# Kernel tuning notes

Measured on AMD Instinct MI355X. Metric: run time of the kernel, lower is better.

## Reference

```python
import jax, jax.numpy as jnp
import numpy as np

B, T, NODES, DEG = 16, 50, 62, 8
IN, C, H, NC, K = 64, 128, 256, 3, 5
G = B * T            # num_graphs
N = G * NODES        # total nodes
E = G * NODES * DEG  # total edges (before self loops)


def setup_inputs() -> dict:
    key = jax.random.key(0)
    ks = jax.random.split(key, 12)
    # random within-graph edges, PyG-batched with node offsets
    rng = np.random.RandomState(0)
    src = rng.randint(0, NODES, size=(G, NODES * DEG))
    dst = rng.randint(0, NODES, size=(G, NODES * DEG))
    off = (np.arange(G) * NODES)[:, None]
    edge_index = jnp.asarray(np.stack([(src + off).ravel(), (dst + off).ravel()]), dtype=jnp.int32)

    def glorot(k, shape, fan_in):
        return jax.random.normal(k, shape, jnp.float32) / np.sqrt(fan_in)

    return {
        "x": jax.random.normal(ks[0], (N, IN), jnp.float32),
        "edge_index": edge_index,
        "edge_attr": jax.random.normal(ks[1], (E, 1), jnp.float32),
        "W_l": glorot(ks[2], (IN, C), IN), "b_l": jnp.zeros((C,), jnp.float32),
        "W_r": glorot(ks[3], (IN, C), IN), "b_r": jnp.zeros((C,), jnp.float32),
        "W_e": glorot(ks[4], (1, C), 1),
        "att": glorot(ks[5], (C,), C),
        "bias_out": jnp.zeros((C,), jnp.float32),
        "W_ih": glorot(ks[6], (3 * H, C), C), "W_hh": glorot(ks[7], (3 * H, H), H),
        "b_ih": jnp.zeros((3 * H,), jnp.float32), "b_hh": jnp.zeros((3 * H,), jnp.float32),
        "W1": glorot(ks[8], (H, H // 2), H), "b1": jnp.zeros((H // 2,), jnp.float32),
        "W2": glorot(ks[9], (H // 2, NC), H // 2), "b2": jnp.zeros((NC,), jnp.float32),
    }


def _forward(x, edge_index, edge_attr, W_l, b_l, W_r, b_r, W_e, att, bias_out,
             W_ih, W_hh, b_ih, b_hh, W1, b1, W2, b2):
    n = x.shape[0]
    src, dst = edge_index[0], edge_index[1]

    # --- GATv2Conv: add self loops with edge_attr fill_value='mean' (PyG default) ---
    sum_attr = jax.ops.segment_sum(edge_attr, dst, num_segments=n)
    cnt = jax.ops.segment_sum(jnp.ones_like(dst, jnp.float32), dst, num_segments=n)
    loop_attr = sum_attr / jnp.clip(cnt, 1.0)[:, None]
    ar = jnp.arange(n, dtype=src.dtype)
    src2 = jnp.concatenate([src, ar])
    dst2 = jnp.concatenate([dst, ar])
    ea = jnp.concatenate([edge_attr, loop_attr], axis=0)

    xl = x @ W_l + b_l          # source-side transform
    xr = x @ W_r + b_r          # target-side transform
    ee = ea @ W_e               # edge embedding (lin_edge, bias=False)

    m = xl[src2] + xr[dst2] + ee                # [E2, C]
    e = jax.nn.leaky_relu(m, 0.2) @ att         # [E2]
    # scatter-softmax over incoming edges per target node (self loops => no empty segs)
    emax = jax.ops.segment_max(e, dst2, num_segments=n)
    ez = jnp.exp(e - emax[dst2])
    den = jax.ops.segment_sum(ez, dst2, num_segments=n)
    alpha = ez / den[dst2]                      # [E2]
    h_sp = jax.ops.segment_sum(alpha[:, None] * xl[src2], dst2, num_segments=n) + bias_out

    # --- mean pool per graph (uniform graph size => reshape) ---
    g = h_sp.reshape(G, NODES, C).mean(axis=1).reshape(B, T, C)

    # --- GRU (PyTorch gate order r, z, n) ---
    def step(h, xt):
        gx = xt @ W_ih.T + b_ih
        gh = h @ W_hh.T + b_hh
        xr_, xz, xn = jnp.split(gx, 3, axis=-1)
        hr, hz, hn = jnp.split(gh, 3, axis=-1)
        r = jax.nn.sigmoid(xr_ + hr)
        z = jax.nn.sigmoid(xz + hz)
        nn_ = jnp.tanh(xn + r * hn)
        h2 = (1.0 - z) * nn_ + z * h
        return h2, h2

    h0 = jnp.zeros((B, H), g.dtype)
    _, hs = jax.lax.scan(step, h0, jnp.swapaxes(g, 0, 1))  # [T,B,H]
    gru_out = jnp.swapaxes(hs, 0, 1)                       # [B,T,H]

    # --- classifier (dropout inactive at eval) ---
    scores = jax.nn.relu(gru_out @ W1 + b1) @ W2 + b2      # [B,T,NC]

    # --- top-k over time per class, then mean over k ---
    vals, idx = jax.lax.top_k(jnp.swapaxes(scores, 1, 2), K)  # [B,NC,K]
    return vals.mean(axis=-1), jnp.swapaxes(idx, 1, 2)        # [B,NC], [B,K,NC]


def reference(x, edge_index, edge_attr, W_l, b_l, W_r, b_r, W_e, att, bias_out,
              W_ih, W_hh, b_ih, b_hh, W1, b1, W2, b2):
    return _forward(x, edge_index, edge_attr, W_l, b_l, W_r, b_r, W_e, att, bias_out,
                    W_ih, W_hh, b_ih, b_hh, W1, b1, W2, b2)
```

## Files before the change

kernel.cpp:

```cpp
#include <hip/hip_runtime.h>
#include <math.h>

#define NNODES 62
#define NDEG 8
#define NGRAPH 800
#define NB 16
#define NT 50
#define NIN 64
#define NCH 128
#define NH 256
#define NCLS 3
#define NTOPK 5
#define NSL 16
#define EPG (NNODES*NDEG)
#define E2G (EPG + NNODES)
#define NTOTAL (NGRAPH*NNODES)
#define ETOTAL (NGRAPH*EPG)

__launch_bounds__(256, 2)
__global__ void k_xrl(const float* __restrict__ x,
                      const float* __restrict__ W_r, const float* __restrict__ b_r,
                      const float* __restrict__ W_l, const float* __restrict__ b_l,
                      float* __restrict__ xr, float* __restrict__ xl) {
    __shared__ __align__(16) float x_s[64 * NIN];
    __shared__ __align__(16) float wr_s[NIN * NCH];
    __shared__ __align__(16) float wl_s[NIN * NCH];
    const int blk = blockIdx.x;
    const int tid = threadIdx.x;
    const int base_v = blk * 64;

    {
        const float4* src = reinterpret_cast<const float4*>(x + (size_t)base_v * NIN);
        float4* dst = reinterpret_cast<float4*>(x_s);
        for (int i = tid; i < 64 * NIN / 4; i += 256) dst[i] = src[i];
        const float4* sr = reinterpret_cast<const float4*>(W_r);
        const float4* sl = reinterpret_cast<const float4*>(W_l);
        float4* dr = reinterpret_cast<float4*>(wr_s);
        float4* dl = reinterpret_cast<float4*>(wl_s);
        for (int i = tid; i < NIN * NCH / 4; i += 256) { dr[i] = sr[i]; dl[i] = sl[i]; }
    }
    __syncthreads();

    const int c4 = (tid & 31) * 4;
    const int ng = tid >> 5;
    float4 aR[8], aL[8];
    float4 br4 = *reinterpret_cast<const float4*>(b_r + c4);
    float4 bl4 = *reinterpret_cast<const float4*>(b_l + c4);
    #pragma unroll
    for (int j = 0; j < 8; ++j) { aR[j] = br4; aL[j] = bl4; }

    const float* xs = x_s + (ng * 8) * NIN;
    for (int k4 = 0; k4 < NIN; k4 += 4) {
        float4 xv[8];
        #pragma unroll
        for (int j = 0; j < 8; ++j)
            xv[j] = *reinterpret_cast<const float4*>(&xs[j * NIN + k4]);
        #pragma unroll
        for (int kk = 0; kk < 4; ++kk) {
            float4 wr = *reinterpret_cast<const float4*>(&wr_s[(k4 + kk) * NCH + c4]);
            float4 wl = *reinterpret_cast<const float4*>(&wl_s[(k4 + kk) * NCH + c4]);
            #pragma unroll
            for (int j = 0; j < 8; ++j) {
                float xk = (kk == 0) ? xv[j].x : (kk == 1) ? xv[j].y
                         : (kk == 2) ? xv[j].z : xv[j].w;
                aR[j].x += xk * wr.x; aR[j].y += xk * wr.y;
                aR[j].z += xk * wr.z; aR[j].w += xk * wr.w;
                aL[j].x += xk * wl.x; aL[j].y += xk * wl.y;
                aL[j].z += xk * wl.z; aL[j].w += xk * wl.w;
            }
        }
    }
    #pragma unroll
    for (int j = 0; j < 8; ++j) {
        int v = base_v + ng * 8 + j;
        *reinterpret_cast<float4*>(xr + (size_t)v * NCH + c4) = aR[j];
        *reinterpret_cast<float4*>(xl + (size_t)v * NCH + c4) = aL[j];
    }
}

__global__ void k_transpose(const float* __restrict__ src, float* __restrict__ dst,
                            int rows, int cols) {
    int idx = blockIdx.x * blockDim.x + threadIdx.x;
    if (idx >= rows * cols) return;
    int r = idx / cols;
    int c = idx - r * cols;
    dst[c * rows + r] = src[idx];
}

__launch_bounds__(256, 4)
__global__ void k_gat(const int* __restrict__ ei, const float* __restrict__ eattr,
                      const float* __restrict__ W_e, const float* __restrict__ att,
                      const float* __restrict__ bias_out,
                      const float* __restrict__ xr_all, const float* __restrict__ xl_all,
                      float* __restrict__ g_all) {
    __shared__ float xl_s[NNODES * NCH];
    __shared__ float e_s[E2G];
    __shared__ unsigned emax_s[NNODES];
    __shared__ float den_s[NNODES];
    __shared__ float la_s[NNODES];
    __shared__ float cnt_s[NNODES];
    __shared__ float sum_s[NNODES];
    __shared__ unsigned short sd_s[EPG];
    __shared__ float attr_s[EPG];
    __shared__ float gacc_s[4 * NCH];

    const int g = blockIdx.x;
    const int tid = threadIdx.x;
    const int base_e = g * EPG;
    const int base_n = g * NNODES;

    for (int v = tid; v < NNODES; v += 256) {
        sum_s[v] = 0.f; cnt_s[v] = 0.f; emax_s[v] = 0u; den_s[v] = 0.f;
    }
    for (int j = tid; j < EPG; j += 256) {
        int s = ei[base_e + j] - base_n;
        int d = ei[ETOTAL + base_e + j] - base_n;
        sd_s[j] = (unsigned short)(s | (d << 6));
        attr_s[j] = eattr[base_e + j];
    }
    {
        const float4* src = reinterpret_cast<const float4*>(xl_all + (size_t)base_n * NCH);
        float4* dst = reinterpret_cast<float4*>(xl_s);
        for (int i = tid; i < NNODES * NCH / 4; i += 256) dst[i] = src[i];
    }
    __syncthreads();

    for (int j = tid; j < EPG; j += 256) {
        int d = sd_s[j] >> 6;
        atomicAdd(&sum_s[d], attr_s[j]);
        atomicAdd(&cnt_s[d], 1.f);
    }
    __syncthreads();
    for (int v = tid; v < NNODES; v += 256) la_s[v] = sum_s[v] / fmaxf(cnt_s[v], 1.f);
    __syncthreads();

    const int wave = tid >> 6;
    const int lane = tid & 63;
    const int grp = lane >> 4;
    const int cb = (lane & 15) * 8;

    float we0[8], at0[8];
    #pragma unroll
    for (int i = 0; i < 8; ++i) { we0[i] = W_e[cb + i]; at0[i] = att[cb + i]; }

    for (int j = wave * 4 + grp; j < E2G; j += 16) {
        int s, d; float a;
        if (j < EPG) { int sd = sd_s[j]; s = sd & 63; d = sd >> 6; a = attr_s[j]; }
        else { s = d = j - EPG; a = la_s[s]; }
        float4 xl0 = *reinterpret_cast<const float4*>(&xl_s[s * NCH + cb]);
        float4 xl1 = *reinterpret_cast<const float4*>(&xl_s[s * NCH + cb + 4]);
        const float* xrp = xr_all + (size_t)(base_n + d) * NCH + cb;
        float4 xr0 = *reinterpret_cast<const float4*>(xrp);
        float4 xr1 = *reinterpret_cast<const float4*>(xrp + 4);
        float m[8] = {xl0.x + xr0.x, xl0.y + xr0.y, xl0.z + xr0.z, xl0.w + xr0.w,
                      xl1.x + xr1.x, xl1.y + xr1.y, xl1.z + xr1.z, xl1.w + xr1.w};
        float t = 0.f;
        #pragma unroll
        for (int i = 0; i < 8; ++i) {
            float mi = m[i] + a * we0[i];
            t += (mi >= 0.f ? mi : 0.2f * mi) * at0[i];
        }
        t += __shfl_xor(t, 1, 64);
        t += __shfl_xor(t, 2, 64);
        t += __shfl_xor(t, 4, 64);
        t += __shfl_xor(t, 8, 64);
        if ((lane & 15) == 0) {
            e_s[j] = t;
            unsigned u = __float_as_uint(t);
            unsigned key = (u & 0x80000000u) ? ~u : (u | 0x80000000u);
            atomicMax(&emax_s[d], key);
        }
    }
    __syncthreads();

    for (int j = tid; j < E2G; j += 256) {
        int d = (j < EPG) ? (sd_s[j] >> 6) : (j - EPG);
        unsigned key = emax_s[d];
        float mx = __uint_as_float((key & 0x80000000u) ? (key & 0x7fffffffu) : ~key);
        float ez = expf(e_s[j] - mx);
        e_s[j] = ez;
        atomicAdd(&den_s[d], ez);
    }
    __syncthreads();
    for (int v = tid; v < NNODES; v += 256) den_s[v] = 1.f / den_s[v];
    __syncthreads();

    float acc[8];
    #pragma unroll
    for (int i = 0; i < 8; ++i) acc[i] = 0.f;
    for (int j = wave * 4 + grp; j < E2G; j += 16) {
        int s, d;
        if (j < EPG) { int sd = sd_s[j]; s = sd & 63; d = sd >> 6; }
        else { s = d = j - EPG; }
        float alpha = e_s[j] * den_s[d];
        float4 x0 = *reinterpret_cast<const float4*>(&xl_s[s * NCH + cb]);
        float4 x1 = *reinterpret_cast<const float4*>(&xl_s[s * NCH + cb + 4]);
        acc[0] += alpha * x0.x; acc[1] += alpha * x0.y;
        acc[2] += alpha * x0.z; acc[3] += alpha * x0.w;
        acc[4] += alpha * x1.x; acc[5] += alpha * x1.y;
        acc[6] += alpha * x1.z; acc[7] += alpha * x1.w;
    }
    #pragma unroll
    for (int i = 0; i < 8; ++i) {
        acc[i] += __shfl_xor(acc[i], 16, 64);
        acc[i] += __shfl_xor(acc[i], 32, 64);
    }
    if (grp == 0) {
        *reinterpret_cast<float4*>(&gacc_s[wave * NCH + cb]) =
            make_float4(acc[0], acc[1], acc[2], acc[3]);
        *reinterpret_cast<float4*>(&gacc_s[wave * NCH + cb + 4]) =
            make_float4(acc[4], acc[5], acc[6], acc[7]);
    }
    __syncthreads();

    for (int c = tid; c < NCH; c += 256) {
        float v = (gacc_s[c] + gacc_s[NCH + c] + gacc_s[2 * NCH + c] + gacc_s[3 * NCH + c])
                      * (1.f / NNODES) + bias_out[c];
        g_all[(size_t)g * NCH + c] = v;
    }
}

__global__ void k_gx(const float* __restrict__ g_all, const float* __restrict__ W_ihT,
                     const float* __restrict__ b_ih, const float* __restrict__ b_hh,
                     float* __restrict__ gx_all, unsigned long long* __restrict__ h_pub) {
    if (blockIdx.x < 32)
        h_pub[(size_t)blockIdx.x * 256 + threadIdx.x] = 0ull;
    int idx = blockIdx.x * blockDim.x + threadIdx.x;
    if (idx >= NGRAPH * 3 * NH) return;
    int gi = idx / (3 * NH);
    int o = idx - gi * (3 * NH);
    float acc = b_ih[o] + (o < 2 * NH ? b_hh[o] : 0.f);
    const float* grow = g_all + (size_t)gi * NCH;
    for (int c = 0; c < NCH; ++c) acc += grow[c] * W_ihT[c * (3 * NH) + o];
    gx_all[idx] = acc;
}

__launch_bounds__(256)
__global__ void k_gru(const float* __restrict__ gx_all, const float* __restrict__ W_hh,
                      const float* __restrict__ b_hh, float* __restrict__ h_all,
                      unsigned long long* __restrict__ h_pub) {
    __shared__ __align__(16) float h_s[NH];
    __shared__ float gh_s[48];
    __shared__ float gx_s[2][48];

    const int bid = blockIdx.x;
    const int b = bid >> 4;
    const int s = bid & 15;
    const int tid = threadIdx.x;
    const int wv = tid >> 6;
    const int g = tid >> 2;
    const int l = tid & 3;

    float4 Wv[16];
    if (tid < 192) {
        int row = (g < 16) ? (NSL * s + g)
                : (g < 32) ? (NH + NSL * s + (g - 16))
                           : (2 * NH + NSL * s + (g - 32));
        const float* wr = W_hh + (size_t)row * NH + 64 * l;
        #pragma unroll
        for (int j = 0; j < 16; ++j) {
            int jeff = (j + 2 * l) & 15;
            Wv[j] = *reinterpret_cast<const float4*>(wr + 4 * jeff);
        }
    }
    const float bhn = (tid < NSL) ? b_hh[2 * NH + NSL * s + tid] : 0.f;
    const int own_lo = NSL * s, own_hi = NSL * s + NSL;

    for (int i = tid; i < NH; i += 256) h_s[i] = 0.f;
    if (wv == 3) {
        int i = tid - 192;
        if (i < 48) {
            int o = (i < 16) ? (NSL * s + i) : (i < 32) ? (NH + NSL * s + i - 16)
                                                        : (2 * NH + NSL * s + i - 32);
            gx_s[0][i] = gx_all[(size_t)(b * NT + 0) * (3 * NH) + o];
        }
    }
    __syncthreads();

    for (int t = 0; t < NT; ++t) {
        if (wv == 3) {
            int i = tid - 192;
            if (i < 48 && t + 1 < NT) {
                int o = (i < 16) ? (NSL * s + i) : (i < 32) ? (NH + NSL * s + i - 16)
                                                            : (2 * NH + NSL * s + i - 32);
                gx_s[(t + 1) & 1][i] = gx_all[(size_t)(b * NT + t + 1) * (3 * NH) + o];
            }
        } else {
            float a0 = 0.f, a1 = 0.f, a2 = 0.f, a3 = 0.f;
            #pragma unroll
            for (int j = 0; j < 16; ++j) {
                int jeff = (j + 2 * l) & 15;
                float4 hv = *reinterpret_cast<const float4*>(&h_s[64 * l + 4 * jeff]);
                float4 w = Wv[j];
                a0 += w.x * hv.x; a1 += w.y * hv.y; a2 += w.z * hv.z; a3 += w.w * hv.w;
            }
            float acc = (a0 + a1) + (a2 + a3);
            acc += __shfl_xor(acc, 1, 64);
            acc += __shfl_xor(acc, 2, 64);
            if (l == 0) gh_s[g] = acc;
        }
        __syncthreads();

        const int par = (t + 1) & 1;
        if (tid < NSL) {
            const float* gx = gx_s[t & 1];
            float r = 1.f / (1.f + expf(-(gx[tid] + gh_s[tid])));
            float z = 1.f / (1.f + expf(-(gx[16 + tid] + gh_s[16 + tid])));
            float n = tanhf(gx[32 + tid] + r * (gh_s[32 + tid] + bhn));
            int o = own_lo + tid;
            float hv = (1.f - z) * n + z * h_s[o];
            h_all[(size_t)(b * NT + t) * NH + o] = hv;
            unsigned long long w = ((unsigned long long)(unsigned)(t + 1) << 32)
                                 | (unsigned long long)__float_as_uint(hv);
            __hip_atomic_store(&h_pub[((size_t)b * 2 + par) * NH + o], w,
                               __ATOMIC_RELAXED, __HIP_MEMORY_SCOPE_AGENT);
            h_s[o] = hv;
        }
        if (tid < own_lo || tid >= own_hi) {
            const unsigned long long* p = &h_pub[((size_t)b * 2 + par) * NH + tid];
            unsigned long long w;
            const unsigned target = (unsigned)(t + 1);
            while ((unsigned)((w = __hip_atomic_load(p, __ATOMIC_RELAXED,
                                                     __HIP_MEMORY_SCOPE_AGENT)) >> 32) != target)
                ;
            h_s[tid] = __uint_as_float((unsigned)w);
        }
        __syncthreads();
    }
}

__launch_bounds__(128)
__global__ void k_cls(const float* __restrict__ h_all,
                      const float* __restrict__ W1, const float* __restrict__ b1,
                      const float* __restrict__ W2, const float* __restrict__ b2,
                      float* __restrict__ sc_all) {
    __shared__ float h_s[NH];
    __shared__ float s1_s[NH / 2];
    const int bt = blockIdx.x;
    const int tid = threadIdx.x;
    h_s[tid] = h_all[(size_t)bt * NH + tid];
    h_s[tid + 128] = h_all[(size_t)bt * NH + tid + 128];
    __syncthreads();
    float acc = b1[tid];
    #pragma unroll 8
    for (int k = 0; k < NH; ++k) acc += h_s[k] * W1[k * (NH / 2) + tid];
    s1_s[tid] = fmaxf(acc, 0.f);
    __syncthreads();
    if (tid < NCLS) {
        float a = b2[tid];
        for (int k = 0; k < NH / 2; ++k) a += s1_s[k] * W2[k * NCLS + tid];
        sc_all[bt * NCLS + tid] = a;
    }
}

__global__ void k_topk(const float* __restrict__ sc_all, float* __restrict__ out) {
    int tid = threadIdx.x;
    if (tid >= NB * NCLS) return;
    int b = tid / NCLS;
    int c = tid - b * NCLS;
    float vals[NT];
    for (int t = 0; t < NT; ++t) vals[t] = sc_all[(b * NT + t) * NCLS + c];
    float sum = 0.f;
    for (int k = 0; k < NTOPK; ++k) {
        float best = -INFINITY; int bi = 0;
        for (int t = 0; t < NT; ++t) {
            if (vals[t] > best) { best = vals[t]; bi = t; }
        }
        vals[bi] = -INFINITY;
        sum += best;
        out[NB * NCLS + b * (NTOPK * NCLS) + k * NCLS + c] = (float)bi;
    }
    out[b * NCLS + c] = sum * (1.f / NTOPK);
}

extern "C" void kernel_launch(void* const* d_in, const int* in_sizes, int n_in,
                              void* d_out, int out_size, void* d_ws, size_t ws_size,
                              hipStream_t stream) {
    const float* x        = (const float*)d_in[0];
    const int*   ei       = (const int*)  d_in[1];
    const float* eattr    = (const float*)d_in[2];
    const float* W_l      = (const float*)d_in[3];
    const float* b_l      = (const float*)d_in[4];
    const float* W_r      = (const float*)d_in[5];
    const float* b_r      = (const float*)d_in[6];
    const float* W_e      = (const float*)d_in[7];
    const float* att      = (const float*)d_in[8];
    const float* bias_out = (const float*)d_in[9];
    const float* W_ih     = (const float*)d_in[10];
    const float* W_hh     = (const float*)d_in[11];
    const float* b_ih     = (const float*)d_in[12];
    const float* b_hh     = (const float*)d_in[13];
    const float* W1       = (const float*)d_in[14];
    const float* b1       = (const float*)d_in[15];
    const float* W2       = (const float*)d_in[16];
    const float* b2       = (const float*)d_in[17];
    float* out = (float*)d_out;

    float* ws = (float*)d_ws;
    float* xr_all = ws;
    float* xl_all = xr_all + (size_t)NTOTAL * NCH;
    float* g_all  = xl_all + (size_t)NTOTAL * NCH;
    float* gx_all = g_all + NGRAPH * NCH;
    float* W_ihT  = gx_all + NGRAPH * 3 * NH;
    float* h_all  = W_ihT + NCH * 3 * NH;
    float* sc_all = h_all + (size_t)NGRAPH * NH;
    unsigned long long* h_pub = (unsigned long long*)xr_all;

    k_xrl<<<NTOTAL / 64, 256, 0, stream>>>(x, W_r, b_r, W_l, b_l, xr_all, xl_all);
    k_transpose<<<(3 * NH * NCH + 255) / 256, 256, 0, stream>>>(W_ih, W_ihT, 3 * NH, NCH);
    k_gat<<<NGRAPH, 256, 0, stream>>>(ei, eattr, W_e, att, bias_out, xr_all, xl_all, g_all);
    k_gx<<<(NGRAPH * 3 * NH + 255) / 256, 256, 0, stream>>>(g_all, W_ihT, b_ih, b_hh, gx_all, h_pub);
    k_gru<<<NB * NSL, 256, 0, stream>>>(gx_all, W_hh, b_hh, h_all, h_pub);
    k_cls<<<NB * NT, 128, 0, stream>>>(h_all, W1, b1, W2, b2, sc_all);
    k_topk<<<1, 64, 0, stream>>>(sc_all, out);
}
```

Baseline: 213.9 us.

## Build per-graph CSR in GAT with online softmax; halve GRU block count

The GAT kernel now builds a destination-sorted CSR in shared memory. Each 16-lane group processes one destination node with an online softmax, which replaces the global atomicMax/atomicAdd passes and several block barriers. The GRU recurrence uses 8 slices of 32 hidden units per batch instead of 16 slices of 16. This halves the number of cross-block spin-wait participants, at the cost of doubling the W_hh register footprint per thread (32 float4). Load imbalance across nodes with different degrees, and register pressure in the GRU, are possible risks.

```diff
diff --git a/kernel.cpp b/kernel.cpp
--- a/kernel.cpp
+++ b/kernel.cpp
@@ -11,7 +11,7 @@
 #define NH 256
 #define NCLS 3
 #define NTOPK 5
-#define NSL 16
+#define NSL 8
 #define EPG (NNODES*NDEG)
 #define E2G (EPG + NNODES)
 #define NTOTAL (NGRAPH*NNODES)
@@ -93,15 +93,15 @@
                       const float* __restrict__ bias_out,
                       const float* __restrict__ xr_all, const float* __restrict__ xl_all,
                       float* __restrict__ g_all) {
-    __shared__ float xl_s[NNODES * NCH];
-    __shared__ float e_s[E2G];
-    __shared__ unsigned emax_s[NNODES];
-    __shared__ float den_s[NNODES];
+    __shared__ __align__(16) float xl_s[NNODES * NCH];
+    __shared__ unsigned short csr_src[E2G];
+    __shared__ float csr_attr[E2G];
+    __shared__ float csr_e[E2G];
+    __shared__ unsigned short off_s[NNODES + 2];
+    __shared__ unsigned cur_s[NNODES];
+    __shared__ unsigned cnt_s[NNODES];
+    __shared__ float asum_s[NNODES];
     __shared__ float la_s[NNODES];
-    __shared__ float cnt_s[NNODES];
-    __shared__ float sum_s[NNODES];
-    __shared__ unsigned short sd_s[EPG];
-    __shared__ float attr_s[EPG];
     __shared__ float gacc_s[4 * NCH];
 
     const int g = blockIdx.x;
@@ -109,103 +109,107 @@
     const int base_e = g * EPG;
     const int base_n = g * NNODES;
 
-    for (int v = tid; v < NNODES; v += 256) {
-        sum_s[v] = 0.f; cnt_s[v] = 0.f; emax_s[v] = 0u; den_s[v] = 0.f;
-    }
-    for (int j = tid; j < EPG; j += 256) {
-        int s = ei[base_e + j] - base_n;
-        int d = ei[ETOTAL + base_e + j] - base_n;
-        sd_s[j] = (unsigned short)(s | (d << 6));
-        attr_s[j] = eattr[base_e + j];
-    }
+    for (int v = tid; v < NNODES; v += 256) { asum_s[v] = 0.f; cnt_s[v] = 0u; cur_s[v] = 0u; }
     {
         const float4* src = reinterpret_cast<const float4*>(xl_all + (size_t)base_n * NCH);
         float4* dst = reinterpret_cast<float4*>(xl_s);
         for (int i = tid; i < NNODES * NCH / 4; i += 256) dst[i] = src[i];
     }
-    __syncthreads();
-
-    for (int j = tid; j < EPG; j += 256) {
-        int d = sd_s[j] >> 6;
-        atomicAdd(&sum_s[d], attr_s[j]);
-        atomicAdd(&cnt_s[d], 1.f);
-    }
-    __syncthreads();
-    for (int v = tid; v < NNODES; v += 256) la_s[v] = sum_s[v] / fmaxf(cnt_s[v], 1.f);
+    int s0 = -1, d0 = 0, s1 = -1, d1 = 0;
+    float a0 = 0.f, a1 = 0.f;
+    {
+        int j0 = tid * 2, j1 = tid * 2 + 1;
+        if (j0 < EPG) { s0 = ei[base_e + j0] - base_n; d0 = ei[ETOTAL + base_e + j0] - base_n; a0 = eattr[base_e + j0]; }
+        if (j1 < EPG) { s1 = ei[base_e + j1] - base_n; d1 = ei[ETOTAL + base_e + j1] - base_n; a1 = eattr[base_e + j1]; }
+    }
+    __syncthreads();
+
+    if (s0 >= 0) { atomicAdd(&cnt_s[d0], 1u); atomicAdd(&asum_s[d0], a0); }
+    if (s1 >= 0) { atomicAdd(&cnt_s[d1], 1u); atomicAdd(&asum_s[d1], a1); }
+    __syncthreads();
+
+    if (tid < 64) {
+        unsigned val = (tid < NNODES) ? (cnt_s[tid] + 1u) : 0u;
+        unsigned xsc = val;
+        #pragma unroll
+        for (int dlt = 1; dlt < 64; dlt <<= 1) {
+            unsigned o = __shfl_up(xsc, dlt, 64);
+            if (tid >= dlt) xsc += o;
+        }
+        if (tid < NNODES) {
+            off_s[tid] = (unsigned short)(xsc - val);
+            la_s[tid] = asum_s[tid] / fmaxf((float)cnt_s[tid], 1.f);
+        }
+        if (tid == NNODES - 1) off_s[NNODES] = (unsigned short)xsc;
+    }
+    __syncthreads();
+
+    if (s0 >= 0) { int sl = off_s[d0] + (int)atomicAdd(&cur_s[d0], 1u); csr_src[sl] = (unsigned short)s0; csr_attr[sl] = a0; }
+    if (s1 >= 0) { int sl = off_s[d1] + (int)atomicAdd(&cur_s[d1], 1u); csr_src[sl] = (unsigned short)s1; csr_attr[sl] = a1; }
+    if (tid < NNODES) { int sl = off_s[tid + 1] - 1; csr_src[sl] = (unsigned short)tid; csr_attr[sl] = la_s[tid]; }
     __syncthreads();
 
     const int wave = tid >> 6;
     const int lane = tid & 63;
-    const int grp = lane >> 4;
-    const int cb = (lane & 15) * 8;
+    const int sub = lane & 15;
+    const int gslot = wave * 4 + (lane >> 4);
+    const int cb = sub * 8;
 
     float we0[8], at0[8];
     #pragma unroll
     for (int i = 0; i < 8; ++i) { we0[i] = W_e[cb + i]; at0[i] = att[cb + i]; }
 
-    for (int j = wave * 4 + grp; j < E2G; j += 16) {
-        int s, d; float a;
-        if (j < EPG) { int sd = sd_s[j]; s = sd & 63; d = sd >> 6; a = attr_s[j]; }
-        else { s = d = j - EPG; a = la_s[s]; }
-        float4 xl0 = *reinterpret_cast<const float4*>(&xl_s[s * NCH + cb]);
-        float4 xl1 = *reinterpret_cast<const float4*>(&xl_s[s * NCH + cb + 4]);
-        const float* xrp = xr_all + (size_t)(base_n + d) * NCH + cb;
-        float4 xr0 = *reinterpret_cast<const float4*>(xrp);
-        float4 xr1 = *reinterpret_cast<const float4*>(xrp + 4);
-        float m[8] = {xl0.x + xr0.x, xl0.y + xr0.y, xl0.z + xr0.z, xl0.w + xr0.w,
-                      xl1.x + xr1.x, xl1.y + xr1.y, xl1.z + xr1.z, xl1.w + xr1.w};
-        float t = 0.f;
-        #pragma unroll
-        for (int i = 0; i < 8; ++i) {
-            float mi = m[i] + a * we0[i];
-            t += (mi >= 0.f ? mi : 0.2f * mi) * at0[i];
-        }
-        t += __shfl_xor(t, 1, 64);
-        t += __shfl_xor(t, 2, 64);
-        t += __shfl_xor(t, 4, 64);
-        t += __shfl_xor(t, 8, 64);
-        if ((lane & 15) == 0) {
-            e_s[j] = t;
-            unsigned u = __float_as_uint(t);
-            unsigned key = (u & 0x80000000u) ? ~u : (u | 0x80000000u);
-            atomicMax(&emax_s[d], key);
-        }
-    }
-    __syncthreads();
-
-    for (int j = tid; j < E2G; j += 256) {
-        int d = (j < EPG) ? (sd_s[j] >> 6) : (j - EPG);
-        unsigned key = emax_s[d];
-        float mx = __uint_as_float((key & 0x80000000u) ? (key & 0x7fffffffu) : ~key);
-        float ez = expf(e_s[j] - mx);
-        e_s[j] = ez;
-        atomicAdd(&den_s[d], ez);
-    }
-    __syncthreads();
-    for (int v = tid; v < NNODES; v += 256) den_s[v] = 1.f / den_s[v];
-    __syncthreads();
-
     float acc[8];
     #pragma unroll
     for (int i = 0; i < 8; ++i) acc[i] = 0.f;
-    for (int j = wave * 4 + grp; j < E2G; j += 16) {
-        int s, d;
-        if (j < EPG) { int sd = sd_s[j]; s = sd & 63; d = sd >> 6; }
-        else { s = d = j - EPG; }
-        float alpha = e_s[j] * den_s[d];
-        float4 x0 = *reinterpret_cast<const float4*>(&xl_s[s * NCH + cb]);
-        float4 x1 = *reinterpret_cast<const float4*>(&xl_s[s * NCH + cb + 4]);
-        acc[0] += alpha * x0.x; acc[1] += alpha * x0.y;
-        acc[2] += alpha * x0.z; acc[3] += alpha * x0.w;
-        acc[4] += alpha * x1.x; acc[5] += alpha * x1.y;
-        acc[6] += alpha * x1.z; acc[7] += alpha * x1.w;
+
+    for (int v = gslot; v < NNODES; v += 16) {
+        const float* xrp = xr_all + (size_t)(base_n + v) * NCH + cb;
+        float4 xr0 = *reinterpret_cast<const float4*>(xrp);
+        float4 xr1 = *reinterpret_cast<const float4*>(xrp + 4);
+        const int lo = off_s[v], hi = off_s[v + 1];
+        float m = -INFINITY, ssum = 0.f;
+        for (int sl = lo; sl < hi; ++sl) {
+            int src = csr_src[sl];
+            float a = csr_attr[sl];
+            float4 x0 = *reinterpret_cast<const float4*>(&xl_s[src * NCH + cb]);
+            float4 x1 = *reinterpret_cast<const float4*>(&xl_s[src * NCH + cb + 4]);
+            float m0, t = 0.f;
+            m0 = x0.x + xr0.x + a * we0[0]; t += (m0 >= 0.f ? m0 : 0.2f * m0) * at0[0];
+            m0 = x0.y + xr0.y + a * we0[1]; t += (m0 >= 0.f ? m0 : 0.2f * m0) * at0[1];
+            m0 = x0.z + xr0.z + a * we0[2]; t += (m0 >= 0.f ? m0 : 0.2f * m0) * at0[2];
+            m0 = x0.w + xr0.w + a * we0[3]; t += (m0 >= 0.f ? m0 : 0.2f * m0) * at0[3];
+            m0 = x1.x + xr1.x + a * we0[4]; t += (m0 >= 0.f ? m0 : 0.2f * m0) * at0[4];
+            m0 = x1.y + xr1.y + a * we0[5]; t += (m0 >= 0.f ? m0 : 0.2f * m0) * at0[5];
+            m0 = x1.z + xr1.z + a * we0[6]; t += (m0 >= 0.f ? m0 : 0.2f * m0) * at0[6];
+            m0 = x1.w + xr1.w + a * we0[7]; t += (m0 >= 0.f ? m0 : 0.2f * m0) * at0[7];
+            t += __shfl_xor(t, 1, 64);
+            t += __shfl_xor(t, 2, 64);
+            t += __shfl_xor(t, 4, 64);
+            t += __shfl_xor(t, 8, 64);
+            if (sub == 0) csr_e[sl] = t;
+            float mn = fmaxf(m, t);
+            ssum = ssum * __expf(m - mn) + __expf(t - mn);
+            m = mn;
+        }
+        float inv = 1.f / ssum;
+        for (int sl = lo; sl < hi; ++sl) {
+            int src = csr_src[sl];
+            float al = __expf(csr_e[sl] - m) * inv;
+            float4 x0 = *reinterpret_cast<const float4*>(&xl_s[src * NCH + cb]);
+            float4 x1 = *reinterpret_cast<const float4*>(&xl_s[src * NCH + cb + 4]);
+            acc[0] += al * x0.x; acc[1] += al * x0.y;
+            acc[2] += al * x0.z; acc[3] += al * x0.w;
+            acc[4] += al * x1.x; acc[5] += al * x1.y;
+            acc[6] += al * x1.z; acc[7] += al * x1.w;
+        }
     }
     #pragma unroll
     for (int i = 0; i < 8; ++i) {
         acc[i] += __shfl_xor(acc[i], 16, 64);
         acc[i] += __shfl_xor(acc[i], 32, 64);
     }
-    if (grp == 0) {
+    if ((lane >> 4) == 0) {
         *reinterpret_cast<float4*>(&gacc_s[wave * NCH + cb]) =
             make_float4(acc[0], acc[1], acc[2], acc[3]);
         *reinterpret_cast<float4*>(&gacc_s[wave * NCH + cb + 4]) =
@@ -240,73 +244,65 @@
                       const float* __restrict__ b_hh, float* __restrict__ h_all,
                       unsigned long long* __restrict__ h_pub) {
     __shared__ __align__(16) float h_s[NH];
-    __shared__ float gh_s[48];
-    __shared__ float gx_s[2][48];
+    __shared__ float gh_s[96];
+    __shared__ float gx_s[2][96];
 
     const int bid = blockIdx.x;
-    const int b = bid >> 4;
-    const int s = bid & 15;
+    const int b = bid >> 3;
+    const int s = bid & 7;
     const int tid = threadIdx.x;
     const int wv = tid >> 6;
-    const int g = tid >> 2;
-    const int l = tid & 3;
-
-    float4 Wv[16];
+    const int g = tid >> 1;
+    const int l = tid & 1;
+
+    float4 Wv[32];
     if (tid < 192) {
-        int row = (g < 16) ? (NSL * s + g)
-                : (g < 32) ? (NH + NSL * s + (g - 16))
-                           : (2 * NH + NSL * s + (g - 32));
-        const float* wr = W_hh + (size_t)row * NH + 64 * l;
+        int row = (g / 32) * NH + 32 * s + (g & 31);
+        const float* wr = W_hh + (size_t)row * NH + 128 * l;
         #pragma unroll
-        for (int j = 0; j < 16; ++j) {
-            int jeff = (j + 2 * l) & 15;
-            Wv[j] = *reinterpret_cast<const float4*>(wr + 4 * jeff);
-        }
-    }
-    const float bhn = (tid < NSL) ? b_hh[2 * NH + NSL * s + tid] : 0.f;
-    const int own_lo = NSL * s, own_hi = NSL * s + NSL;
+        for (int j = 0; j < 32; ++j) Wv[j] = *reinterpret_cast<const float4*>(wr + 4 * j);
+    }
+    const float bhn = (tid < 32) ? b_hh[2 * NH + 32 * s + tid] : 0.f;
+    const int own_lo = 32 * s, own_hi = own_lo + 32;
 
     for (int i = tid; i < NH; i += 256) h_s[i] = 0.f;
     if (wv == 3) {
         int i = tid - 192;
-        if (i < 48) {
-            int o = (i < 16) ? (NSL * s + i) : (i < 32) ? (NH + NSL * s + i - 16)
-                                                        : (2 * NH + NSL * s + i - 32);
-            gx_s[0][i] = gx_all[(size_t)(b * NT + 0) * (3 * NH) + o];
-        }
+        int o = (i < 32) ? (32 * s + i) : (NH + 32 * s + (i - 32));
+        gx_s[0][i] = gx_all[(size_t)(b * NT) * (3 * NH) + o];
+        if (i < 32) gx_s[0][i + 64] = gx_all[(size_t)(b * NT) * (3 * NH) + 2 * NH + 32 * s + i];
     }
     __syncthreads();
 
     for (int t = 0; t < NT; ++t) {
+        const int par = (t + 1) & 1;
         if (wv == 3) {
             int i = tid - 192;
-            if (i < 48 && t + 1 < NT) {
-                int o = (i < 16) ? (NSL * s + i) : (i < 32) ? (NH + NSL * s + i - 16)
-                                                            : (2 * NH + NSL * s + i - 32);
-                gx_s[(t + 1) & 1][i] = gx_all[(size_t)(b * NT + t + 1) * (3 * NH) + o];
+            if (t + 1 < NT) {
+                size_t base = (size_t)(b * NT + t + 1) * (3 * NH);
+                int o = (i < 32) ? (32 * s + i) : (NH + 32 * s + (i - 32));
+                gx_s[par][i] = gx_all[base + o];
+                if (i < 32) gx_s[par][i + 64] = gx_all[base + 2 * NH + 32 * s + i];
             }
         } else {
             float a0 = 0.f, a1 = 0.f, a2 = 0.f, a3 = 0.f;
             #pragma unroll
-            for (int j = 0; j < 16; ++j) {
-                int jeff = (j + 2 * l) & 15;
-                float4 hv = *reinterpret_cast<const float4*>(&h_s[64 * l + 4 * jeff]);
+            for (int j = 0; j < 32; ++j) {
+                float4 hv = *reinterpret_cast<const float4*>(&h_s[128 * l + 4 * j]);
                 float4 w = Wv[j];
                 a0 += w.x * hv.x; a1 += w.y * hv.y; a2 += w.z * hv.z; a3 += w.w * hv.w;
             }
             float acc = (a0 + a1) + (a2 + a3);
             acc += __shfl_xor(acc, 1, 64);
-            acc += __shfl_xor(acc, 2, 64);
             if (l == 0) gh_s[g] = acc;
         }
         __syncthreads();
 
-        const int par = (t + 1) & 1;
-        if (tid < NSL) {
+        if (tid < 32) {
             const float* gx = gx_s[t & 1];
             float r = 1.f / (1.f + expf(-(gx[tid] + gh_s[tid])));
-            float z = 1.f / (1.f + expf(-(gx[16 + tid] + gh_s[16 + tid])));
-            float n = tanhf(gx[32 + tid] + r * (gh_s[32 + tid] + bhn));
+            float z = 1.f / (1.f + expf(-(gx[32 + tid] + gh_s[32 + tid])));
+            float n = tanhf(gx[64 + tid] + r * (gh_s[64 + tid] + bhn));
             int o = own_lo + tid;
             float hv = (1.f - z) * n + z * h_s[o];
             h_all[(size_t)(b * NT + t) * NH + o] = hv;
```

New measurement: 227.4 us. 6.3% more time.
